# Performance work log

Hardware: AMD Instinct MI355X
Metric: run time of the kernel (lower is better)

Reference implementation:

```python
import jax, jax.numpy as jnp
import numpy as np

EPS = 1e-6
FEAT = 1024
HEADS = 16
HDIM = FEAT // HEADS
FF = 500


def setup_inputs() -> dict:
    key = jax.random.key(0)
    ks = jax.random.split(key, 12)
    B, S = 4, 2048
    inp = {
        "x": jax.random.normal(ks[0], (B, S, FEAT), jnp.float32),
        "mask": jax.random.randint(ks[1], (B, S, S), 0, 2, jnp.int32),
        "alpha1": jnp.ones((FEAT,), jnp.float32),
        "bias1": jnp.zeros((FEAT,), jnp.float32),
        "alpha2": jnp.ones((FEAT,), jnp.float32),
        "bias2": jnp.zeros((FEAT,), jnp.float32),
        "Wq": jax.random.normal(ks[2], (FEAT, FEAT), jnp.float32) * (1.0 / np.sqrt(FEAT)),
        "bq": jnp.zeros((FEAT,), jnp.float32),
        "Wk": jax.random.normal(ks[3], (FEAT, FEAT), jnp.float32) * (1.0 / np.sqrt(FEAT)),
        "bk": jnp.zeros((FEAT,), jnp.float32),
        "Wv": jax.random.normal(ks[4], (FEAT, FEAT), jnp.float32) * (1.0 / np.sqrt(FEAT)),
        "bv": jnp.zeros((FEAT,), jnp.float32),
        "Wo": jax.random.normal(ks[5], (FEAT, FEAT), jnp.float32) * (1.0 / np.sqrt(FEAT)),
        "bo": jnp.zeros((FEAT,), jnp.float32),
        "W1": jax.random.normal(ks[6], (FEAT, FF), jnp.float32) * (1.0 / np.sqrt(FEAT)),
        "b1": jnp.zeros((FF,), jnp.float32),
        "W2": jax.random.normal(ks[7], (FF, FEAT), jnp.float32) * (1.0 / np.sqrt(FF)),
        "b2": jnp.zeros((FEAT,), jnp.float32),
    }
    return inp


def _norm(x, alpha, bias):
    m = jnp.mean(x, axis=-1, keepdims=True)
    # torch.std uses Bessel's correction (ddof=1)
    s = jnp.std(x, axis=-1, keepdims=True, ddof=1)
    return alpha * (x - m) / (s + EPS) + bias


def _attn(x2, mask, Wq, bq, Wk, bk, Wv, bv, Wo, bo):
    B, S, _ = x2.shape
    q = (x2 @ Wq + bq).reshape(B, S, HEADS, HDIM)
    k = (x2 @ Wk + bk).reshape(B, S, HEADS, HDIM)
    v = (x2 @ Wv + bv).reshape(B, S, HEADS, HDIM)
    scores = jnp.einsum("bqhd,bkhd->bhqk", q, k) / np.sqrt(HDIM).astype(np.float32)
    # faithful to source: masked positions filled with -1e-09 (not -1e9)
    scores = jnp.where(mask[:, None, :, :] == 0, jnp.float32(-1e-09), scores)
    probs = jax.nn.softmax(scores, axis=-1)
    out = jnp.einsum("bhqk,bkhd->bqhd", probs, v).reshape(B, S, FEAT)
    return out @ Wo + bo


def reference(x, mask, alpha1, bias1, alpha2, bias2, Wq, bq, Wk, bk, Wv, bv, Wo, bo, W1, b1, W2, b2):
    x2 = _norm(x, alpha1, bias1)
    x = x + _attn(x2, mask, Wq, bq, Wk, bk, Wv, bv, Wo, bo)
    x2 = _norm(x, alpha2, bias2)
    h = jax.nn.elu(x2 @ W1 + b1)
    x = x + (h @ W2 + b2)
    return x
```

## Files before the change

kernel.cpp:

```cpp
#include <hip/hip_runtime.h>
#include <hip/hip_bf16.h>
#include <math.h>

#define BATCH 4
#define SEQ 2048
#define FEAT 1024
#define HEADS 16
#define HDIM 64
#define FF 500
#define FFP 512
#define ROWS (BATCH * SEQ)
#define QKVSTR 3072
#define AQ 128

typedef unsigned short ushortT;
typedef __attribute__((ext_vector_type(8))) short short8;
typedef __attribute__((ext_vector_type(4))) float floatx4;

#if defined(__has_builtin) && __has_builtin(__builtin_amdgcn_exp2f)
#define EXP2F(x) __builtin_amdgcn_exp2f(x)
#else
#define EXP2F(x) exp2f(x)
#endif

__device__ __forceinline__ unsigned short f2bf(float f) {
    unsigned int u = __builtin_bit_cast(unsigned int, f);
    u += 0x7fffu + ((u >> 16) & 1u);
    return (unsigned short)(u >> 16);
}
__device__ __forceinline__ float bf2f(short b) {
    unsigned int u = ((unsigned int)(unsigned short)b) << 16;
    return __builtin_bit_cast(float, u);
}

__device__ __forceinline__ void async16(void* lds, const void* g) {
    __builtin_amdgcn_global_load_lds(
        (const __attribute__((address_space(1))) unsigned int*)g,
        (__attribute__((address_space(3))) unsigned int*)lds, 16, 0, 0);
}

__global__ void prep_kernel(const float* __restrict__ Wq, const float* __restrict__ Wk,
                            const float* __restrict__ Wv, const float* __restrict__ Wo,
                            const float* __restrict__ W1, const float* __restrict__ W2,
                            const float* __restrict__ bq, const float* __restrict__ bk,
                            const float* __restrict__ bv, const float* __restrict__ b1,
                            ushortT* __restrict__ Wqkvt, ushortT* __restrict__ Wot,
                            ushortT* __restrict__ W1t, ushortT* __restrict__ W2t,
                            float* __restrict__ bqkv, float* __restrict__ b1p)
{
    const int t = blockIdx.x;
    const int tid = threadIdx.x;
    if (t == 1280) {
        for (int i = tid; i < QKVSTR; i += 256)
            bqkv[i] = (i < 1024) ? bq[i] : ((i < 2048) ? bk[i - 1024] : bv[i - 2048]);
        for (int i = tid; i < FFP; i += 256)
            b1p[i] = (i < FF) ? b1[i] : 0.0f;
        return;
    }
    const float* W; ushortT* Wt; int K, N, Kp, bx, by;
    if (t < 1024) {
        const int wi = t >> 8, lt = t & 255;
        bx = lt & 15; by = lt >> 4; K = FEAT; N = FEAT; Kp = FEAT;
        W  = (wi == 0) ? Wq : (wi == 1) ? Wk : (wi == 2) ? Wv : Wo;
        Wt = (wi == 3) ? Wot : (Wqkvt + (size_t)wi * FEAT * FEAT);
    } else if (t < 1152) {
        const int lt = t - 1024; bx = lt & 7; by = lt >> 3;
        K = FEAT; N = FF; Kp = FEAT; W = W1; Wt = W1t;
    } else {
        const int lt = t - 1152; bx = lt & 15; by = lt >> 4;
        K = FF; N = FEAT; Kp = FFP; W = W2; Wt = W2t;
    }

    __shared__ float T[64][65];
    const int n0 = bx * 64, k0 = by * 64;
    const int r = tid >> 4;
    const int c = (tid & 15) * 4;
    #pragma unroll
    for (int i = 0; i < 4; i++) {
        const int kk = k0 + r + i * 16;
        #pragma unroll
        for (int e = 0; e < 4; e++) {
            const int nn = n0 + c + e;
            T[r + i * 16][c + e] = (kk < K && nn < N) ? W[(size_t)kk * N + nn] : 0.0f;
        }
    }
    __syncthreads();
    #pragma unroll
    for (int i = 0; i < 4; i++) {
        const int nn = r + i * 16;
        ushort4 o;
        o.x = f2bf(T[c + 0][nn]);
        o.y = f2bf(T[c + 1][nn]);
        o.z = f2bf(T[c + 2][nn]);
        o.w = f2bf(T[c + 3][nn]);
        *(ushort4*)(Wt + (size_t)(n0 + nn) * Kp + k0 + c) = o;
    }
}

__global__ void maskbits_kernel(const int* __restrict__ mask,
                                unsigned int* __restrict__ bits)
{
    const size_t g = (size_t)blockIdx.x * 256 + threadIdx.x;
    const int lane = threadIdx.x & 63;
    const unsigned long long bal = __ballot(mask[g] != 0);
    if (lane == 0)  bits[g >> 5] = (unsigned int)bal;
    if (lane == 32) bits[g >> 5] = (unsigned int)(bal >> 32);
}

__global__ void ln_kernel(const float* __restrict__ x,
                          const float* __restrict__ alpha,
                          const float* __restrict__ bias,
                          ushortT* __restrict__ out)
{
    __shared__ float p1[4], p2[4];
    const int row = blockIdx.x;
    const int tid = threadIdx.x;
    const int wave = tid >> 6, lane = tid & 63;
    float4 v = ((const float4*)(x + (size_t)row * FEAT))[tid];

    float s1 = v.x + v.y + v.z + v.w;
    float s2 = v.x * v.x + v.y * v.y + v.z * v.z + v.w * v.w;
    #pragma unroll
    for (int off = 32; off > 0; off >>= 1) {
        s1 += __shfl_xor(s1, off);
        s2 += __shfl_xor(s2, off);
    }
    if (lane == 0) { p1[wave] = s1; p2[wave] = s2; }
    __syncthreads();
    const float t1 = p1[0] + p1[1] + p1[2] + p1[3];
    const float t2 = p2[0] + p2[1] + p2[2] + p2[3];
    const float mean = t1 * (1.0f / 1024.0f);
    const float var = fmaxf(t2 - 1024.0f * mean * mean, 0.0f) * (1.0f / 1023.0f);
    const float inv = 1.0f / (sqrtf(var) + 1e-6f);

    const float4 a = ((const float4*)alpha)[tid];
    const float4 b = ((const float4*)bias)[tid];
    ushort4 o;
    o.x = f2bf(a.x * (v.x - mean) * inv + b.x);
    o.y = f2bf(a.y * (v.y - mean) * inv + b.y);
    o.z = f2bf(a.z * (v.z - mean) * inv + b.z);
    o.w = f2bf(a.w * (v.w - mean) * inv + b.w);
    ((ushort4*)(out + (size_t)row * FEAT))[tid] = o;
}

template<int ACT, int RES, int OUT_BF16, int BN>
__global__ __launch_bounds__(256)
void mfma_gemm(const ushortT* __restrict__ A, const ushortT* __restrict__ Bt,
               const float* __restrict__ bias, const float* __restrict__ R,
               void* __restrict__ Cout, int M, int N, int K)
{
    constexpr int MT = (BN == 128) ? 4 : 2;
    constexpr int MSPAN = (BN == 128) ? 64 : 32;
    __shared__ ushortT As[2][128 * 32];
    __shared__ ushortT Bs[2][BN * 32];

    const int tid  = threadIdx.x;
    const int wave = tid >> 6, lane = tid & 63;
    const int quad = lane >> 4, l16 = lane & 15;
    const int wm = (BN == 128) ? (wave >> 1) : wave;
    const int wn = (BN == 128) ? (wave & 1) : 0;
    const int row0 = blockIdx.y * 128, col0 = blockIdx.x * BN;

    const floatx4 z4 = {0.f, 0.f, 0.f, 0.f};
    floatx4 acc[MT][4];
    #pragma unroll
    for (int i = 0; i < MT; i++)
        #pragma unroll
        for (int j = 0; j < 4; j++) acc[i][j] = z4;

    for (int k0 = 0; k0 < K; k0 += 64) {
        __syncthreads();
        #pragma unroll
        for (int kh = 0; kh < 2; kh++) {
            #pragma unroll
            for (int i = 0; i < 2; i++) {
                const int rbase = 16 * (wave + 4 * i);
                const int r = rbase + (lane >> 2);
                const int co = (lane & 3) * 8;
                async16((char*)As[kh] + rbase * 64,
                        A + (size_t)(row0 + r) * K + k0 + kh * 32 + co);
            }
            if (BN == 128) {
                #pragma unroll
                for (int i = 0; i < 2; i++) {
                    const int rbase = 16 * (wave + 4 * i);
                    const int r = rbase + (lane >> 2);
                    const int co = (lane & 3) * 8;
                    async16((char*)Bs[kh] + rbase * 64,
                            Bt + (size_t)(col0 + r) * K + k0 + kh * 32 + co);
                }
            } else {
                const int rbase = 16 * wave;
                const int r = rbase + (lane >> 2);
                const int co = (lane & 3) * 8;
                async16((char*)Bs[kh] + rbase * 64,
                        Bt + (size_t)(col0 + r) * K + k0 + kh * 32 + co);
            }
        }
        __syncthreads();

        #pragma unroll
        for (int kh = 0; kh < 2; kh++) {
            short8 af[MT], bf[4];
            #pragma unroll
            for (int mt = 0; mt < MT; mt++)
                af[mt] = *(const short8*)&As[kh][(MSPAN * wm + 16 * mt + l16) * 32 + quad * 8];
            #pragma unroll
            for (int nt = 0; nt < 4; nt++)
                bf[nt] = *(const short8*)&Bs[kh][(64 * wn + 16 * nt + l16) * 32 + quad * 8];
            #pragma unroll
            for (int mt = 0; mt < MT; mt++)
                #pragma unroll
                for (int nt = 0; nt < 4; nt++)
                    acc[mt][nt] = __builtin_amdgcn_mfma_f32_16x16x32_bf16(
                        af[mt], bf[nt], acc[mt][nt], 0, 0, 0);
        }
    }

    #pragma unroll
    for (int mt = 0; mt < MT; mt++) {
        #pragma unroll
        for (int nt = 0; nt < 4; nt++) {
            const int col = col0 + 64 * wn + 16 * nt + l16;
            #pragma unroll
            for (int r = 0; r < 4; r++) {
                const int row = row0 + MSPAN * wm + 16 * mt + quad * 4 + r;
                float val = acc[mt][nt][r] + bias[col];
                if (ACT == 1) val = (val > 0.0f) ? val : (__expf(val) - 1.0f);
                if (RES) val += R[(size_t)row * N + col];
                if (OUT_BF16)
                    ((ushortT*)Cout)[(size_t)row * N + col] = f2bf(val);
                else
                    ((float*)Cout)[(size_t)row * N + col] = val;
            }
        }
    }
}

__global__ void transpose_v_kernel(const ushortT* __restrict__ v, ushortT* __restrict__ vt)
{
    __shared__ ushortT T[64][80];
    const int bid = blockIdx.x;
    const int jt = bid & 31, h = (bid >> 5) & 15, b = bid >> 9;
    const int j0 = jt * 64;
    const int tid = threadIdx.x;

    const int j = tid >> 2;
    #pragma unroll
    for (int i = 0; i < 2; i++) {
        const int c = (tid & 3) * 2 + i;
        short8 val = *(const short8*)(v + (size_t)(b * SEQ + j0 + j) * QKVSTR + h * 64 + c * 8);
        *(short8*)&T[j][c * 8] = val;
    }
    __syncthreads();
    const int d = tid >> 2;
    #pragma unroll
    for (int i = 0; i < 2; i++) {
        const int cj = (tid & 3) * 2 + i;
        union { short8 v8; ushortT u[8]; } tmp;
        #pragma unroll
        for (int e = 0; e < 8; e++) tmp.u[e] = T[cj * 8 + e][d];
        *(short8*)(vt + ((size_t)((b * HEADS + h) * 64 + d)) * SEQ + j0 + cj * 8) = tmp.v8;
    }
}

__global__ __launch_bounds__(512)
void mfma_attn(const ushortT* __restrict__ qkv, const ushortT* __restrict__ vt,
               const unsigned int* __restrict__ mbits, ushortT* __restrict__ attn_out)
{
    __shared__ ushortT Ks[2][64 * 64];
    __shared__ ushortT Vts[2][64 * 64];
    __shared__ ushortT Ps[AQ * 64];

    const int tid = threadIdx.x;
    const int wave = tid >> 6, lane = tid & 63;
    const int quad = lane >> 4, l16 = lane & 15;
    const int bid = ((blockIdx.x & 7) << 7) | (blockIdx.x >> 3);
    const int qt = bid & 15, h = (bid >> 4) & 15, b = bid >> 8;
    const int q0 = qt * AQ;

    const ushortT* qptr = qkv;
    const ushortT* kptr = qkv + 1024;

    short8 qf[2];
    {
        const size_t qrow = (size_t)(b * SEQ + q0 + 16 * wave + l16);
        short8 t0 = *(const short8*)(qptr + qrow * QKVSTR + h * 64 + quad * 8);
        short8 t1 = *(const short8*)(qptr + qrow * QKVSTR + h * 64 + 32 + quad * 8);
        const float cs = 0.125f * 1.4426950408889634f;
        #pragma unroll
        for (int i = 0; i < 8; i++) {
            qf[0][i] = (short)f2bf(bf2f(t0[i]) * cs);
            qf[1][i] = (short)f2bf(bf2f(t1[i]) * cs);
        }
    }

    short8 ones8;
    #pragma unroll
    for (int i = 0; i < 8; i++) ones8[i] = (short)0x3F80;

    const floatx4 z4 = {0.f, 0.f, 0.f, 0.f};
    floatx4 o[4];
    #pragma unroll
    for (int dt = 0; dt < 4; dt++) o[dt] = z4;
    floatx4 lacc = z4;

    const int rr = tid >> 3;
    const int c0 = tid & 7;
    const ushortT* gk = kptr + (size_t)(b * SEQ + rr) * QKVSTR + h * 64 + c0 * 8;
    const ushortT* gv = vt + ((size_t)((b * HEADS + h) * 64 + rr)) * SEQ + c0 * 8;
    short8 rk, rv;

#define ATTN_ISSUE() {                                                       \
    rk = *(const short8*)gk;                                                 \
    rv = *(const short8*)gv;                                                 \
    gk += (size_t)64 * QKVSTR; gv += 64; }

#define ATTN_WRITE(BI) {                                                     \
    *(short8*)&Ks[BI][rr * 64 + ((c0 ^ (rr & 7)) * 8)] = rk;                 \
    *(short8*)&Vts[BI][rr * 64 + ((c0 ^ (rr & 7)) * 8)] = rv; }

    const unsigned int* mrowp =
        mbits + (size_t)(b * SEQ + q0 + 16 * wave + l16) * (SEQ / 32);
    const int mloc = 16 * wave + l16;

    ATTN_ISSUE();
    ATTN_WRITE(0);
    unsigned int w0 = mrowp[0], w1 = mrowp[1];

    #pragma unroll 2
    for (int jt = 0; jt < 32; jt++) {
        __syncthreads();
        const int cur = jt & 1;
        unsigned int wn0, wn1;
        if (jt < 31) {
            ATTN_ISSUE();
            wn0 = mrowp[jt * 2 + 2];
            wn1 = mrowp[jt * 2 + 3];
        }

        floatx4 st[4];
        __builtin_amdgcn_s_setprio(1);
        #pragma unroll
        for (int nt = 0; nt < 4; nt++) {
            const int j = nt * 16 + l16;
            short8 ka0 = *(const short8*)&Ks[cur][j * 64 + ((quad ^ (j & 7)) * 8)];
            short8 ka1 = *(const short8*)&Ks[cur][j * 64 + (((4 + quad) ^ (j & 7)) * 8)];
            floatx4 t = z4;
            t = __builtin_amdgcn_mfma_f32_16x16x32_bf16(ka0, qf[0], t, 0, 0, 0);
            t = __builtin_amdgcn_mfma_f32_16x16x32_bf16(ka1, qf[1], t, 0, 0, 0);
            st[nt] = t;
        }
        __builtin_amdgcn_s_setprio(0);

        #pragma unroll
        for (int nt = 0; nt < 4; nt++) {
            const unsigned int ww = (nt & 2) ? w1 : w0;
            const unsigned int wsh = ww >> ((nt & 1) * 16 + quad * 4);
            float p[4];
            p[0] = EXP2F((wsh & 1u) ? st[nt][0] : 0.0f);
            p[1] = EXP2F((wsh & 2u) ? st[nt][1] : 0.0f);
            p[2] = EXP2F((wsh & 4u) ? st[nt][2] : 0.0f);
            p[3] = EXP2F((wsh & 8u) ? st[nt][3] : 0.0f);
            const int j0 = nt * 16 + quad * 4;
            const int chunk = (j0 >> 3) ^ (mloc & 7);
            const int ci = j0 & 7;
            ushortT* dst = &Ps[mloc * 64 + chunk * 8 + ci];
            *(__hip_bfloat162*)(dst)     = __float22bfloat162_rn(make_float2(p[0], p[1]));
            *(__hip_bfloat162*)(dst + 2) = __float22bfloat162_rn(make_float2(p[2], p[3]));
        }

        short8 pa0 = *(const short8*)&Ps[mloc * 64 + ((quad ^ (mloc & 7)) * 8)];
        short8 pa1 = *(const short8*)&Ps[mloc * 64 + (((4 + quad) ^ (mloc & 7)) * 8)];
        lacc = __builtin_amdgcn_mfma_f32_16x16x32_bf16(pa0, ones8, lacc, 0, 0, 0);
        lacc = __builtin_amdgcn_mfma_f32_16x16x32_bf16(pa1, ones8, lacc, 0, 0, 0);
        __builtin_amdgcn_s_setprio(1);
        #pragma unroll
        for (int dt = 0; dt < 4; dt++) {
            const int d = dt * 16 + l16;
            short8 vb0 = *(const short8*)&Vts[cur][d * 64 + ((quad ^ (d & 7)) * 8)];
            short8 vb1 = *(const short8*)&Vts[cur][d * 64 + (((4 + quad) ^ (d & 7)) * 8)];
            o[dt] = __builtin_amdgcn_mfma_f32_16x16x32_bf16(pa0, vb0, o[dt], 0, 0, 0);
            o[dt] = __builtin_amdgcn_mfma_f32_16x16x32_bf16(pa1, vb1, o[dt], 0, 0, 0);
        }
        __builtin_amdgcn_s_setprio(0);

        if (jt < 31) {
            ATTN_WRITE(cur ^ 1);
            w0 = wn0; w1 = wn1;
        }
    }

    #pragma unroll
    for (int r = 0; r < 4; r++) {
        const float inv_l = 1.0f / lacc[r];
        const size_t row = (size_t)(b * SEQ + q0 + 16 * wave + quad * 4 + r);
        #pragma unroll
        for (int dt = 0; dt < 4; dt++) {
            attn_out[row * FEAT + h * 64 + dt * 16 + l16] = f2bf(o[dt][r] * inv_l);
        }
    }
#undef ATTN_ISSUE
#undef ATTN_WRITE
}

extern "C" void kernel_launch(void* const* d_in, const int* in_sizes, int n_in,
                              void* d_out, int out_size, void* d_ws, size_t ws_size,
                              hipStream_t stream)
{
    const float* x      = (const float*)d_in[0];
    const int*   mask   = (const int*)d_in[1];
    const float* alpha1 = (const float*)d_in[2];
    const float* bias1  = (const float*)d_in[3];
    const float* alpha2 = (const float*)d_in[4];
    const float* bias2  = (const float*)d_in[5];
    const float* Wq     = (const float*)d_in[6];
    const float* bq     = (const float*)d_in[7];
    const float* Wk     = (const float*)d_in[8];
    const float* bk     = (const float*)d_in[9];
    const float* Wv     = (const float*)d_in[10];
    const float* bv     = (const float*)d_in[11];
    const float* Wo     = (const float*)d_in[12];
    const float* bo     = (const float*)d_in[13];
    const float* W1     = (const float*)d_in[14];
    const float* b1     = (const float*)d_in[15];
    const float* W2     = (const float*)d_in[16];
    const float* b2     = (const float*)d_in[17];
    float* out = (float*)d_out;

    char* ws = (char*)d_ws;
    const size_t MB = 1024 * 1024;
    ushortT* x2b    = (ushortT*)(ws);
    ushortT* attn_o = (ushortT*)(ws);
    ushortT* qkv    = (ushortT*)(ws + 16 * MB);
    ushortT* x2b2   = (ushortT*)(ws + 16 * MB);
    ushortT* hbuf   = (ushortT*)(ws + 32 * MB);
    ushortT* vtb    = (ushortT*)(ws + 64 * MB);
    ushortT* Wqkvt  = (ushortT*)(ws + 80 * MB);
    ushortT* Wot    = (ushortT*)(ws + 86 * MB);
    ushortT* W1t    = (ushortT*)(ws + 88 * MB);
    ushortT* W2t    = (ushortT*)(ws + 89 * MB);
    float*   b1p    = (float*)  (ws + 90 * MB);
    float*   bqkv   = (float*)  (ws + 90 * MB + 16384);
    unsigned int* mbits = (unsigned int*)(ws + 91 * MB);

    const dim3 blk(256);

    prep_kernel<<<1281, blk, 0, stream>>>(Wq, Wk, Wv, Wo, W1, W2, bq, bk, bv, b1,
                                          Wqkvt, Wot, W1t, W2t, bqkv, b1p);
    maskbits_kernel<<<(BATCH * SEQ * SEQ) / 256, blk, 0, stream>>>(mask, mbits);

    ln_kernel<<<ROWS, blk, 0, stream>>>(x, alpha1, bias1, x2b);

    mfma_gemm<0, 0, 1, 128><<<dim3(24, 64), blk, 0, stream>>>(
        x2b, Wqkvt, bqkv, nullptr, qkv, ROWS, QKVSTR, FEAT);

    transpose_v_kernel<<<BATCH * HEADS * (SEQ / 64), blk, 0, stream>>>(qkv + 2048, vtb);
    mfma_attn<<<BATCH * HEADS * (SEQ / AQ), dim3(512), 0, stream>>>(qkv, vtb, mbits, attn_o);

    mfma_gemm<0, 1, 0, 128><<<dim3(8, 64), blk, 0, stream>>>(
        attn_o, Wot, bo, x, out, ROWS, FEAT, FEAT);

    ln_kernel<<<ROWS, blk, 0, stream>>>(out, alpha2, bias2, x2b2);

    mfma_gemm<1, 0, 1, 64><<<dim3(FFP / 64, 64), blk, 0, stream>>>(
        x2b2, W1t, b1p, nullptr, hbuf, ROWS, FFP, FEAT);

    mfma_gemm<0, 1, 0, 128><<<dim3(8, 64), blk, 0, stream>>>(
        hbuf, W2t, b2, out, out, ROWS, FEAT, FFP);
}
```

Measured before the change: 459.6 us.

## Remap GEMM block order across XCDs and single-buffer attention K/V LDS

The GEMM kernel remaps its linear block id so consecutive tiles are grouped per XCD (stride-8 interleave), aiming for better L2 locality of shared A/B panels. The attention kernel drops the double-buffered K/V shared memory in favour of a single buffer. Each iteration now writes the prefetched registers and adds a second barrier before compute. This halves that LDS footprint, which may raise occupancy, but it serialises the store with compute and adds a sync per tile.

```diff
diff --git a/kernel.cpp b/kernel.cpp
--- a/kernel.cpp
+++ b/kernel.cpp
@@ -159,7 +159,12 @@
     const int quad = lane >> 4, l16 = lane & 15;
     const int wm = (BN == 128) ? (wave >> 1) : wave;
     const int wn = (BN == 128) ? (wave & 1) : 0;
-    const int row0 = blockIdx.y * 128, col0 = blockIdx.x * BN;
+
+    const int nbx = gridDim.x;
+    int lid = blockIdx.y * nbx + blockIdx.x;
+    const int cpx = (nbx * gridDim.y) >> 3;
+    lid = (lid & 7) * cpx + (lid >> 3);
+    const int row0 = (lid / nbx) * 128, col0 = (lid % nbx) * BN;
 
     const floatx4 z4 = {0.f, 0.f, 0.f, 0.f};
     floatx4 acc[MT][4];
@@ -268,8 +273,8 @@
 void mfma_attn(const ushortT* __restrict__ qkv, const ushortT* __restrict__ vt,
                const unsigned int* __restrict__ mbits, ushortT* __restrict__ attn_out)
 {
-    __shared__ ushortT Ks[2][64 * 64];
-    __shared__ ushortT Vts[2][64 * 64];
+    __shared__ ushortT Ks[64 * 64];
+    __shared__ ushortT Vts[64 * 64];
     __shared__ ushortT Ps[AQ * 64];
 
     const int tid = threadIdx.x;
@@ -316,23 +321,23 @@
     rv = *(const short8*)gv;                                                 \
     gk += (size_t)64 * QKVSTR; gv += 64; }
 
-#define ATTN_WRITE(BI) {                                                     \
-    *(short8*)&Ks[BI][rr * 64 + ((c0 ^ (rr & 7)) * 8)] = rk;                 \
-    *(short8*)&Vts[BI][rr * 64 + ((c0 ^ (rr & 7)) * 8)] = rv; }
+#define ATTN_WRITE() {                                                       \
+    *(short8*)&Ks[rr * 64 + ((c0 ^ (rr & 7)) * 8)] = rk;                     \
+    *(short8*)&Vts[rr * 64 + ((c0 ^ (rr & 7)) * 8)] = rv; }
 
     const unsigned int* mrowp =
         mbits + (size_t)(b * SEQ + q0 + 16 * wave + l16) * (SEQ / 32);
     const int mloc = 16 * wave + l16;
 
     ATTN_ISSUE();
-    ATTN_WRITE(0);
     unsigned int w0 = mrowp[0], w1 = mrowp[1];
 
     #pragma unroll 2
     for (int jt = 0; jt < 32; jt++) {
         __syncthreads();
-        const int cur = jt & 1;
-        unsigned int wn0, wn1;
+        ATTN_WRITE();
+        __syncthreads();
+        unsigned int wn0 = 0, wn1 = 0;
         if (jt < 31) {
             ATTN_ISSUE();
             wn0 = mrowp[jt * 2 + 2];
@@ -344,8 +349,8 @@
         #pragma unroll
         for (int nt = 0; nt < 4; nt++) {
             const int j = nt * 16 + l16;
-            short8 ka0 = *(const short8*)&Ks[cur][j * 64 + ((quad ^ (j & 7)) * 8)];
-            short8 ka1 = *(const short8*)&Ks[cur][j * 64 + (((4 + quad) ^ (j & 7)) * 8)];
+            short8 ka0 = *(const short8*)&Ks[j * 64 + ((quad ^ (j & 7)) * 8)];
+            short8 ka1 = *(const short8*)&Ks[j * 64 + (((4 + quad) ^ (j & 7)) * 8)];
             floatx4 t = z4;
             t = __builtin_amdgcn_mfma_f32_16x16x32_bf16(ka0, qf[0], t, 0, 0, 0);
             t = __builtin_amdgcn_mfma_f32_16x16x32_bf16(ka1, qf[1], t, 0, 0, 0);
@@ -378,17 +383,14 @@
         #pragma unroll
         for (int dt = 0; dt < 4; dt++) {
             const int d = dt * 16 + l16;
-            short8 vb0 = *(const short8*)&Vts[cur][d * 64 + ((quad ^ (d & 7)) * 8)];
-            short8 vb1 = *(const short8*)&Vts[cur][d * 64 + (((4 + quad) ^ (d & 7)) * 8)];
+            short8 vb0 = *(const short8*)&Vts[d * 64 + ((quad ^ (d & 7)) * 8)];
+            short8 vb1 = *(const short8*)&Vts[d * 64 + (((4 + quad) ^ (d & 7)) * 8)];
             o[dt] = __builtin_amdgcn_mfma_f32_16x16x32_bf16(pa0, vb0, o[dt], 0, 0, 0);
             o[dt] = __builtin_amdgcn_mfma_f32_16x16x32_bf16(pa1, vb1, o[dt], 0, 0, 0);
         }
         __builtin_amdgcn_s_setprio(0);
 
-        if (jt < 31) {
-            ATTN_WRITE(cur ^ 1);
-            w0 = wn0; w1 = wn1;
-        }
+        if (jt < 31) { w0 = wn0; w1 = wn1; }
     }
 
     #pragma unroll
```

New measurement: 459.5 us. No clear change (-0.0%).
